# Optimization experiments

Hardware: AMD Instinct MI355X
Metric: run time of the kernel (lower is better)

Reference implementation:

```python
import jax, jax.numpy as jnp
import numpy as np

HIDDEN = 128
N_NODES = 50000
N_EDGES = 600000
EPS = 1e-5


def setup_inputs() -> dict:
    key = jax.random.key(0)
    ks = jax.random.split(key, 10)
    x = jax.random.normal(ks[0], (N_NODES, HIDDEN), dtype=jnp.float32)
    edge_index = jax.random.randint(ks[1], (2, N_EDGES), 0, N_NODES, dtype=jnp.int64)
    edge_type = jax.random.randint(ks[2], (N_EDGES,), 0, 3, dtype=jnp.int64)
    s = 0.02
    # Stacked per-type message weights: [3, 2H, H] (types 0=power, 1=comm, 2=cross)
    Wmsg = jax.random.normal(ks[3], (3, 2 * HIDDEN, HIDDEN), dtype=jnp.float32) * s
    bmsg = jnp.zeros((3, HIDDEN), dtype=jnp.float32)
    Wupd = jax.random.normal(ks[4], (2 * HIDDEN, HIDDEN), dtype=jnp.float32) * s
    bupd = jnp.zeros((HIDDEN,), dtype=jnp.float32)
    gamma = jnp.ones((HIDDEN,), dtype=jnp.float32)
    beta = jnp.zeros((HIDDEN,), dtype=jnp.float32)
    return {
        "x": x, "edge_index": edge_index, "edge_type": edge_type,
        "Wmsg": Wmsg, "bmsg": bmsg, "Wupd": Wupd, "bupd": bupd,
        "gamma": gamma, "beta": beta,
    }


def reference(x, edge_index, edge_type, Wmsg, bmsg, Wupd, bupd, gamma, beta):
    src, dst = edge_index[0], edge_index[1]
    N = x.shape[0]
    E = edge_type.shape[0]
    # Typed-edge gather + linear message: [E, 2H]
    msg_input = jnp.concatenate([x[src], x[dst]], axis=-1)
    # Compute all 3 typed linears, then select per-edge type: [E, 3, H] -> [E, H]
    all_msgs = jnp.einsum('ec,tch->eth', msg_input, Wmsg) + bmsg
    messages = jnp.take_along_axis(all_msgs, edge_type[:, None, None], axis=1)[:, 0]
    # scatter_add aggregation + count-normalize (count clamped to >= 1)
    agg = jax.ops.segment_sum(messages, dst, num_segments=N)
    count = jax.ops.segment_sum(jnp.ones((E, 1), dtype=x.dtype), dst, num_segments=N)
    agg = agg / jnp.maximum(count, 1.0)
    # Update MLP: Linear -> LayerNorm -> GELU (Dropout is identity in eval)
    h = jnp.concatenate([x, agg], axis=-1) @ Wupd + bupd
    mu = jnp.mean(h, axis=-1, keepdims=True)
    var = jnp.var(h, axis=-1, keepdims=True)
    hn = (h - mu) / jnp.sqrt(var + EPS) * gamma + beta
    x_updated = jax.nn.gelu(hn, approximate=False)
    return x + x_updated
```

## Files before the change

kernel.cpp:

```cpp
#include <hip/hip_runtime.h>
#include <hip/hip_bf16.h>
#include <math.h>

#define HIDDEN 128
#define NNODES 50000
#define NEDGES 600000
#define EPS 1e-5f
#define SCAN_CHUNK 1024
#define NSCAN_BLOCKS ((NNODES + SCAN_CHUNK - 1) / SCAN_CHUNK)
#define MPAD 50048

#define P0_W6T_END   384
#define P0_BV_END    387
#define P0_WUT_END   515
#define P0_XB_END    (515 + 6256)
#define P0_HIST_END  (P0_XB_END + 2344)

#define OFF_W6T  ((size_t)0)
#define OFF_BV   ((size_t)196608)
#define OFF_WUT  ((size_t)199680)
#define OFF_XB   ((size_t)265216)
#define OFF_ABB  ((size_t)13077504)
#define OFF_AGB  ((size_t)51477504)
#define OFF_HIST ((size_t)64289792)
#define OFF_EXCL ((size_t)64489984)
#define OFF_CURS ((size_t)64690176)
#define OFF_BSUM ((size_t)64890368)
#define OFF_PACK ((size_t)64890624)

typedef __attribute__((ext_vector_type(8))) short bf16x8;
typedef __attribute__((ext_vector_type(4))) float f32x4;

__device__ inline unsigned short f2bf(float f) {
    union { float f; unsigned u; } c; c.f = f;
    unsigned u = c.u;
    u += 0x7FFF + ((u >> 16) & 1);
    return (unsigned short)(u >> 16);
}
__device__ inline float bf2f(unsigned short h) {
    union { unsigned u; float f; } c; c.u = ((unsigned)h) << 16;
    return c.f;
}

__device__ inline unsigned char f2fp8(float f) {
    int d = __builtin_amdgcn_cvt_pk_fp8_f32(f, f, 0, false);
    return (unsigned char)(d & 0xFF);
}
template <int S>
__device__ inline float fp8f(unsigned q) {
    return __builtin_amdgcn_cvt_f32_fp8(q, S);
}

__global__ __launch_bounds__(256) void phase0(const float* __restrict__ Wmsg,
                                              const float* __restrict__ bmsg,
                                              const float* __restrict__ Wupd,
                                              const float* __restrict__ x,
                                              const int* __restrict__ ei,
                                              unsigned short* __restrict__ W6T,
                                              float* __restrict__ Bv,
                                              unsigned short* __restrict__ WuT,
                                              unsigned short* __restrict__ Xb,
                                              int* __restrict__ hist) {
    const int b = blockIdx.x;
    const int tid = threadIdx.x;
    if (b < P0_W6T_END) {
        int idx = b * 256 + tid;
        int col = idx >> 7;
        int k = idx & 127;
        int half = col >= 384;
        int rem = col - half * 384;
        int t = rem >> 7;
        int h = rem & 127;
        W6T[idx] = f2bf(Wmsg[t * 32768 + (half * 128 + k) * 128 + h]);
    } else if (b < P0_BV_END) {
        int idx = (b - P0_W6T_END) * 256 + tid;
        if (idx < 768) Bv[idx] = (idx < 384) ? 0.f : bmsg[idx - 384];
    } else if (b < P0_WUT_END) {
        int idx = (b - P0_BV_END) * 256 + tid;
        int n = idx >> 8;
        int k = idx & 255;
        WuT[idx] = f2bf(Wupd[(size_t)k * 128 + n]);
    } else if (b < P0_XB_END) {
        int i = (b - P0_WUT_END) * 256 + tid;
        int base = i * 4;
        if (base < MPAD * 128) {
            ushort4 o;
            if (base < NNODES * 128) {
                float4 v = *(const float4*)(x + base);
                o.x = f2bf(v.x); o.y = f2bf(v.y); o.z = f2bf(v.z); o.w = f2bf(v.w);
            } else {
                o.x = o.y = o.z = o.w = 0;
            }
            *(ushort4*)(Xb + base) = o;
        }
    } else {
        int e = (b - P0_XB_END) * 256 + tid;
        if (e < NEDGES) atomicAdd(&hist[ei[NEDGES + e]], 1);
    }
}

__global__ __launch_bounds__(256) void gemm_ab(const unsigned short* __restrict__ Xb,
                                               const unsigned short* __restrict__ W6T,
                                               const float* __restrict__ Bv,
                                               unsigned char* __restrict__ ABb8) {
    __shared__ unsigned char lds_buf[64 * 272];
    const int tid = threadIdx.x;
    const int mbase = blockIdx.x * 64;
    const int w = tid >> 6;
    const int nbase = blockIdx.y * 256 + w * 64;
    const int lane = tid & 63;
    const int r = lane & 15;
    const int quad = lane >> 4;

    bf16x8 b[4][4];
#pragma unroll
    for (int ks = 0; ks < 4; ++ks)
#pragma unroll
        for (int ni = 0; ni < 4; ++ni)
            b[ks][ni] = *(const bf16x8*)(W6T + (size_t)(nbase + ni * 16 + r) * 128 + ks * 32 + quad * 8);

    unsigned short* xs = (unsigned short*)lds_buf;
#pragma unroll
    for (int i = 0; i < 4; ++i) {
        int item = i * 256 + tid;
        int row = item >> 4;
        int kb = item & 15;
        bf16x8 v = *(const bf16x8*)(Xb + (size_t)(mbase + row) * 128 + kb * 8);
        *(bf16x8*)&xs[row * 128 + ((kb ^ (row & 7)) * 8)] = v;
    }
    __syncthreads();

    f32x4 acc[4][4];
#pragma unroll
    for (int mi = 0; mi < 4; ++mi)
#pragma unroll
        for (int ni = 0; ni < 4; ++ni) acc[mi][ni] = (f32x4){0.f, 0.f, 0.f, 0.f};

#pragma unroll
    for (int ks = 0; ks < 4; ++ks) {
        bf16x8 a[4];
        const int kb = ks * 4 + quad;
#pragma unroll
        for (int mi = 0; mi < 4; ++mi)
            a[mi] = *(const bf16x8*)&xs[(mi * 16 + r) * 128 + ((kb ^ (r & 7)) * 8)];
#pragma unroll
        for (int mi = 0; mi < 4; ++mi)
#pragma unroll
            for (int ni = 0; ni < 4; ++ni)
                acc[mi][ni] = __builtin_amdgcn_mfma_f32_16x16x32_bf16(a[mi], b[ks][ni], acc[mi][ni], 0, 0, 0);
    }

    __syncthreads();
    unsigned char (*tile)[272] = (unsigned char(*)[272])lds_buf;

#pragma unroll
    for (int ni = 0; ni < 4; ++ni) {
        const int col_l = w * 64 + ni * 16 + r;
        const float bias = Bv[blockIdx.y * 256 + col_l];
#pragma unroll
        for (int mi = 0; mi < 4; ++mi) {
            f32x4 v = acc[mi][ni];
#pragma unroll
            for (int reg = 0; reg < 4; ++reg) {
                tile[mi * 16 + quad * 4 + reg][col_l] = f2fp8(v[reg] + bias);
            }
        }
    }
    __syncthreads();

#pragma unroll
    for (int i = 0; i < 4; ++i) {
        int item = i * 256 + tid;
        int row_l = item >> 4;
        int chunk = item & 15;
        int grow = mbase + row_l;
        if (grow < NNODES) {
            uint4 v = *(const uint4*)&tile[row_l][chunk * 16];
            *(uint4*)(ABb8 + (size_t)grow * 768 + blockIdx.y * 256 + chunk * 16) = v;
        }
    }
}

__global__ __launch_bounds__(256) void scan_phase1(const int* __restrict__ hist,
                                                   int* __restrict__ excl,
                                                   int* __restrict__ blockSums) {
    __shared__ int lds[256];
    const int blk = blockIdx.x;
    const int t = threadIdx.x;
    const int base = blk * SCAN_CHUNK + t * 4;
    int v[4];
    int s = 0;
#pragma unroll
    for (int i = 0; i < 4; ++i) {
        v[i] = (base + i < NNODES) ? hist[base + i] : 0;
        s += v[i];
    }
    lds[t] = s;
    __syncthreads();
    for (int off = 1; off < 256; off <<= 1) {
        int add = (t >= off) ? lds[t - off] : 0;
        __syncthreads();
        lds[t] += add;
        __syncthreads();
    }
    int incl = lds[t];
    int run = incl - s;
#pragma unroll
    for (int i = 0; i < 4; ++i) {
        if (base + i < NNODES) excl[base + i] = run;
        run += v[i];
    }
    if (t == 255) blockSums[blk] = incl;
}

__global__ __launch_bounds__(256) void scan_phase3(int* __restrict__ excl,
                                                   const int* __restrict__ blockSums,
                                                   int* __restrict__ cursor) {
    __shared__ int s_add;
    const int blk = blockIdx.x;
    const int t = threadIdx.x;
    if (t < 64) {
        int v = (t < blk) ? blockSums[t] : 0;
#pragma unroll
        for (int off = 32; off >= 1; off >>= 1) v += __shfl_xor(v, off, 64);
        if (t == 0) s_add = v;
    }
    __syncthreads();
    const int add = s_add;
    for (int i = t; i < SCAN_CHUNK; i += 256) {
        int idx = blk * SCAN_CHUNK + i;
        if (idx < NNODES) {
            int o = excl[idx] + add;
            excl[idx] = o;
            cursor[idx] = o;
        }
    }
}

__global__ __launch_bounds__(256) void edge_bucket(const int* __restrict__ ei,
                                                   const int* __restrict__ et,
                                                   int* __restrict__ cursor,
                                                   unsigned* __restrict__ packed) {
    int e = blockIdx.x * 256 + threadIdx.x;
    if (e >= NEDGES) return;
    int src = ei[e];
    int dst = ei[NEDGES + e];
    int t = et[e];
    int pos = atomicAdd(&cursor[dst], 1);
    packed[pos] = (unsigned)(src * 192 + t * 32) | ((unsigned)t << 25);
}

__global__ __launch_bounds__(256) void aggregate(const unsigned* __restrict__ packed,
                                                 const int* __restrict__ excl,
                                                 const int* __restrict__ hist,
                                                 const unsigned char* __restrict__ ABb8,
                                                 unsigned short* __restrict__ Agb) {
    const int n = blockIdx.x * 4 + (threadIdx.x >> 6);
    const int lane = threadIdx.x & 63;
    if (n >= NNODES) return;
    const int start = excl[n];
    const int deg = hist[n];
    const unsigned* ABu = (const unsigned*)ABb8;

    const int half = lane >> 5;
    const int cl = lane & 31;

    float s0 = 0.f, s1 = 0.f, s2 = 0.f, s3 = 0.f;
    int c1 = 0, c2 = 0;

    for (int base = 0; base < deg; base += 64) {
        const int m = min(64, deg - base);
        unsigned v = 0;
        if (lane < m) v = packed[start + base + lane];
        int j = 0;
        for (; j + 8 <= m; j += 8) {
            unsigned e0 = __shfl(v, j + 0 + half, 64);
            unsigned e1 = __shfl(v, j + 2 + half, 64);
            unsigned e2 = __shfl(v, j + 4 + half, 64);
            unsigned e3 = __shfl(v, j + 6 + half, 64);
            unsigned q0 = ABu[(e0 & 0x1FFFFFF) + cl];
            unsigned q1 = ABu[(e1 & 0x1FFFFFF) + cl];
            unsigned q2 = ABu[(e2 & 0x1FFFFFF) + cl];
            unsigned q3 = ABu[(e3 & 0x1FFFFFF) + cl];
            int t0 = e0 >> 25, t1 = e1 >> 25, t2 = e2 >> 25, t3 = e3 >> 25;
            c1 += (t0 == 1) + (t1 == 1) + (t2 == 1) + (t3 == 1);
            c2 += (t0 == 2) + (t1 == 2) + (t2 == 2) + (t3 == 2);
            s0 += (fp8f<0>(q0) + fp8f<0>(q1)) + (fp8f<0>(q2) + fp8f<0>(q3));
            s1 += (fp8f<1>(q0) + fp8f<1>(q1)) + (fp8f<1>(q2) + fp8f<1>(q3));
            s2 += (fp8f<2>(q0) + fp8f<2>(q1)) + (fp8f<2>(q2) + fp8f<2>(q3));
            s3 += (fp8f<3>(q0) + fp8f<3>(q1)) + (fp8f<3>(q2) + fp8f<3>(q3));
        }
        for (; j + 2 <= m; j += 2) {
            unsigned e0 = __shfl(v, j + half, 64);
            unsigned q0 = ABu[(e0 & 0x1FFFFFF) + cl];
            int t0 = e0 >> 25;
            c1 += (t0 == 1);
            c2 += (t0 == 2);
            s0 += fp8f<0>(q0); s1 += fp8f<1>(q0);
            s2 += fp8f<2>(q0); s3 += fp8f<3>(q0);
        }
        if (j < m) {
            unsigned e0 = __shfl(v, j, 64);
            if (half == 0) {
                unsigned q0 = ABu[(e0 & 0x1FFFFFF) + cl];
                int t0 = e0 >> 25;
                c1 += (t0 == 1);
                c2 += (t0 == 2);
                s0 += fp8f<0>(q0); s1 += fp8f<1>(q0);
                s2 += fp8f<2>(q0); s3 += fp8f<3>(q0);
            }
        }
    }

    s0 += __shfl_xor(s0, 32, 64);
    s1 += __shfl_xor(s1, 32, 64);
    s2 += __shfl_xor(s2, 32, 64);
    s3 += __shfl_xor(s3, 32, 64);
    c1 += __shfl_xor(c1, 32, 64);
    c2 += __shfl_xor(c2, 32, 64);
    const int c0 = deg - c1 - c2;

    const unsigned* brow = ABu + (size_t)n * 192 + 96;
    if (c0) {
        unsigned p = brow[cl];
        s0 += c0 * fp8f<0>(p); s1 += c0 * fp8f<1>(p);
        s2 += c0 * fp8f<2>(p); s3 += c0 * fp8f<3>(p);
    }
    if (c1) {
        unsigned p = brow[32 + cl];
        s0 += c1 * fp8f<0>(p); s1 += c1 * fp8f<1>(p);
        s2 += c1 * fp8f<2>(p); s3 += c1 * fp8f<3>(p);
    }
    if (c2) {
        unsigned p = brow[64 + cl];
        s0 += c2 * fp8f<0>(p); s1 += c2 * fp8f<1>(p);
        s2 += c2 * fp8f<2>(p); s3 += c2 * fp8f<3>(p);
    }

    const float inv = 1.0f / fmaxf((float)deg, 1.0f);
    if (half == 0) {
        uint2 o;
        o.x = (unsigned)f2bf(s0 * inv) | ((unsigned)f2bf(s1 * inv) << 16);
        o.y = (unsigned)f2bf(s2 * inv) | ((unsigned)f2bf(s3 * inv) << 16);
        ((uint2*)(Agb + (size_t)n * 128))[cl] = o;
    }
}

__global__ __launch_bounds__(256, 4) void update_mfma(const unsigned short* __restrict__ Xb,
                                                      const unsigned short* __restrict__ Agb,
                                                      const unsigned short* __restrict__ WuT,
                                                      const float* __restrict__ bupd,
                                                      const float* __restrict__ gamma,
                                                      const float* __restrict__ beta,
                                                      float* __restrict__ out) {
    __shared__ float sred[4][2][16];

    const int tid = threadIdx.x;
    const int w = tid >> 6;
    const int lane = tid & 63;
    const int r = lane & 15;
    const int quad = lane >> 4;
    const int rowbase = blockIdx.x * 16;

    bf16x8 a[8];
#pragma unroll
    for (int ks = 0; ks < 4; ++ks)
        a[ks] = *(const bf16x8*)(Xb + (size_t)(rowbase + r) * 128 + ks * 32 + quad * 8);
#pragma unroll
    for (int ks = 4; ks < 8; ++ks)
        a[ks] = *(const bf16x8*)(Agb + (size_t)(rowbase + r) * 128 + (ks - 4) * 32 + quad * 8);

    bf16x8 e0, e1;
#pragma unroll
    for (int t = 0; t < 8; ++t) {
        e0[t] = (short)((quad * 8 + t == r) ? 0x3F80 : 0);
        e1[t] = (short)((quad * 8 + t == 16 + r) ? 0x3F80 : 0);
    }
    f32x4 xr[2];
#pragma unroll
    for (int nl = 0; nl < 2; ++nl) {
        f32x4 z = (f32x4){0.f, 0.f, 0.f, 0.f};
        xr[nl] = __builtin_amdgcn_mfma_f32_16x16x32_bf16(a[w], nl ? e1 : e0, z, 0, 0, 0);
    }

    f32x4 acc[2];
#pragma unroll
    for (int nl = 0; nl < 2; ++nl) acc[nl] = (f32x4){0.f, 0.f, 0.f, 0.f};

#pragma unroll
    for (int ks = 0; ks < 8; ++ks) {
        const int kb = ks * 4 + quad;
#pragma unroll
        for (int nl = 0; nl < 2; ++nl) {
            bf16x8 b = *(const bf16x8*)(WuT + (size_t)((w * 2 + nl) * 16 + r) * 256 + kb * 8);
            acc[nl] = __builtin_amdgcn_mfma_f32_16x16x32_bf16(a[ks], b, acc[nl], 0, 0, 0);
        }
    }

    float vals[2][4];
    float gcol[2], bcol[2];
#pragma unroll
    for (int nl = 0; nl < 2; ++nl) {
        const int col = (w * 2 + nl) * 16 + r;
        const float bias = bupd[col];
        gcol[nl] = gamma[col];
        bcol[nl] = beta[col];
#pragma unroll
        for (int reg = 0; reg < 4; ++reg) vals[nl][reg] = acc[nl][reg] + bias;
    }

#pragma unroll
    for (int reg = 0; reg < 4; ++reg) {
        float s = vals[0][reg] + vals[1][reg];
        float s2 = vals[0][reg] * vals[0][reg] + vals[1][reg] * vals[1][reg];
#pragma unroll
        for (int off = 8; off >= 1; off >>= 1) {
            s += __shfl_xor(s, off, 64);
            s2 += __shfl_xor(s2, off, 64);
        }
        if (r == 0) {
            sred[w][0][quad * 4 + reg] = s;
            sred[w][1][quad * 4 + reg] = s2;
        }
    }
    __syncthreads();

#pragma unroll
    for (int reg = 0; reg < 4; ++reg) {
        const int rowL = quad * 4 + reg;
        const float s = (sred[0][0][rowL] + sred[1][0][rowL]) + (sred[2][0][rowL] + sred[3][0][rowL]);
        const float s2 = (sred[0][1][rowL] + sred[1][1][rowL]) + (sred[2][1][rowL] + sred[3][1][rowL]);
        const int row = rowbase + rowL;
        if (row < NNODES) {
            const float mu = s * (1.0f / 128.0f);
            const float var = s2 * (1.0f / 128.0f) - mu * mu;
            const float inv = rsqrtf(var + EPS);
#pragma unroll
            for (int nl = 0; nl < 2; ++nl) {
                const int col = (w * 2 + nl) * 16 + r;
                float hn = (vals[nl][reg] - mu) * inv * gcol[nl] + bcol[nl];
                float ge = 0.5f * hn * (1.0f + erff(hn * 0.70710678118654752f));
                out[(size_t)row * 128 + col] = xr[nl][reg] + ge;
            }
        }
    }
}

extern "C" void kernel_launch(void* const* d_in, const int* in_sizes, int n_in,
                              void* d_out, int out_size, void* d_ws, size_t ws_size,
                              hipStream_t stream) {
    const float* x     = (const float*)d_in[0];
    const int*   ei    = (const int*)d_in[1];
    const int*   et    = (const int*)d_in[2];
    const float* Wmsg  = (const float*)d_in[3];
    const float* bmsg  = (const float*)d_in[4];
    const float* Wupd  = (const float*)d_in[5];
    const float* bupd  = (const float*)d_in[6];
    const float* gamma = (const float*)d_in[7];
    const float* beta  = (const float*)d_in[8];
    float* out = (float*)d_out;

    char* ws = (char*)d_ws;
    unsigned short* W6T  = (unsigned short*)(ws + OFF_W6T);
    float*          Bv   = (float*)(ws + OFF_BV);
    unsigned short* WuT  = (unsigned short*)(ws + OFF_WUT);
    unsigned short* Xb   = (unsigned short*)(ws + OFF_XB);
    unsigned char*  ABb8 = (unsigned char*)(ws + OFF_ABB);
    unsigned short* Agb  = (unsigned short*)(ws + OFF_AGB);
    int*            hist = (int*)(ws + OFF_HIST);
    int*            excl = (int*)(ws + OFF_EXCL);
    int*            curs = (int*)(ws + OFF_CURS);
    int*            bsum = (int*)(ws + OFF_BSUM);
    unsigned*       pack = (unsigned*)(ws + OFF_PACK);

    (void)hipMemsetAsync(hist, 0, NNODES * sizeof(int), stream);

    phase0<<<P0_HIST_END, 256, 0, stream>>>(Wmsg, bmsg, Wupd, x, ei, W6T, Bv, WuT, Xb, hist);
    gemm_ab<<<dim3(MPAD / 64, 3), 256, 0, stream>>>(Xb, W6T, Bv, ABb8);
    scan_phase1<<<NSCAN_BLOCKS, 256, 0, stream>>>(hist, excl, bsum);
    scan_phase3<<<NSCAN_BLOCKS, 256, 0, stream>>>(excl, bsum, curs);
    edge_bucket<<<(NEDGES + 255) / 256, 256, 0, stream>>>(ei, et, curs, pack);
    aggregate<<<(NNODES + 3) / 4, 256, 0, stream>>>(pack, excl, hist, ABb8, Agb);
    update_mfma<<<MPAD / 16, 256, 0, stream>>>(Xb, Agb, WuT, bupd, gamma, beta, out);
}
```

Before: 259.4 us.

## Make update kernel persistent with register-resident weights over 8 waves

The update GEMM+LayerNorm+GELU kernel becomes a persistent grid of 512 blocks with 512 threads. Each of the 8 waves owns one 16-column slice and keeps its Wupd^T fragment in registers, then loops over 16-row tiles. Weights and bias/gamma/beta are no longer reloaded for every tile, and a double-buffered shared reduction array allows one barrier per tile. The cost is fewer independent blocks for hiding latency and an 8-way cross-wave reduction per tile, and the A fragments are still loaded redundantly by each wave.

```diff
diff --git a/kernel.cpp b/kernel.cpp
--- a/kernel.cpp
+++ b/kernel.cpp
@@ -9,6 +9,7 @@
 #define SCAN_CHUNK 1024
 #define NSCAN_BLOCKS ((NNODES + SCAN_CHUNK - 1) / SCAN_CHUNK)
 #define MPAD 50048
+#define NTILES (MPAD / 16)
 
 #define P0_W6T_END   384
 #define P0_BV_END    387
@@ -346,101 +347,93 @@
     }
 }
 
-__global__ __launch_bounds__(256, 4) void update_mfma(const unsigned short* __restrict__ Xb,
+__global__ __launch_bounds__(512, 4) void update_mfma(const unsigned short* __restrict__ Xb,
                                                       const unsigned short* __restrict__ Agb,
                                                       const unsigned short* __restrict__ WuT,
                                                       const float* __restrict__ bupd,
                                                       const float* __restrict__ gamma,
                                                       const float* __restrict__ beta,
                                                       float* __restrict__ out) {
-    __shared__ float sred[4][2][16];
+    __shared__ float sred[2][8][2][16];
 
     const int tid = threadIdx.x;
     const int w = tid >> 6;
     const int lane = tid & 63;
     const int r = lane & 15;
     const int quad = lane >> 4;
-    const int rowbase = blockIdx.x * 16;
-
-    bf16x8 a[8];
-#pragma unroll
-    for (int ks = 0; ks < 4; ++ks)
-        a[ks] = *(const bf16x8*)(Xb + (size_t)(rowbase + r) * 128 + ks * 32 + quad * 8);
-#pragma unroll
-    for (int ks = 4; ks < 8; ++ks)
-        a[ks] = *(const bf16x8*)(Agb + (size_t)(rowbase + r) * 128 + (ks - 4) * 32 + quad * 8);
-
-    bf16x8 e0, e1;
-#pragma unroll
-    for (int t = 0; t < 8; ++t) {
-        e0[t] = (short)((quad * 8 + t == r) ? 0x3F80 : 0);
-        e1[t] = (short)((quad * 8 + t == 16 + r) ? 0x3F80 : 0);
-    }
-    f32x4 xr[2];
-#pragma unroll
-    for (int nl = 0; nl < 2; ++nl) {
-        f32x4 z = (f32x4){0.f, 0.f, 0.f, 0.f};
-        xr[nl] = __builtin_amdgcn_mfma_f32_16x16x32_bf16(a[w], nl ? e1 : e0, z, 0, 0, 0);
-    }
-
-    f32x4 acc[2];
-#pragma unroll
-    for (int nl = 0; nl < 2; ++nl) acc[nl] = (f32x4){0.f, 0.f, 0.f, 0.f};
-
-#pragma unroll
-    for (int ks = 0; ks < 8; ++ks) {
-        const int kb = ks * 4 + quad;
-#pragma unroll
-        for (int nl = 0; nl < 2; ++nl) {
-            bf16x8 b = *(const bf16x8*)(WuT + (size_t)((w * 2 + nl) * 16 + r) * 256 + kb * 8);
-            acc[nl] = __builtin_amdgcn_mfma_f32_16x16x32_bf16(a[ks], b, acc[nl], 0, 0, 0);
-        }
-    }
-
-    float vals[2][4];
-    float gcol[2], bcol[2];
-#pragma unroll
-    for (int nl = 0; nl < 2; ++nl) {
-        const int col = (w * 2 + nl) * 16 + r;
-        const float bias = bupd[col];
-        gcol[nl] = gamma[col];
-        bcol[nl] = beta[col];
-#pragma unroll
-        for (int reg = 0; reg < 4; ++reg) vals[nl][reg] = acc[nl][reg] + bias;
-    }
-
-#pragma unroll
-    for (int reg = 0; reg < 4; ++reg) {
-        float s = vals[0][reg] + vals[1][reg];
-        float s2 = vals[0][reg] * vals[0][reg] + vals[1][reg] * vals[1][reg];
-#pragma unroll
-        for (int off = 8; off >= 1; off >>= 1) {
-            s += __shfl_xor(s, off, 64);
-            s2 += __shfl_xor(s2, off, 64);
-        }
-        if (r == 0) {
-            sred[w][0][quad * 4 + reg] = s;
-            sred[w][1][quad * 4 + reg] = s2;
-        }
-    }
-    __syncthreads();
-
-#pragma unroll
-    for (int reg = 0; reg < 4; ++reg) {
-        const int rowL = quad * 4 + reg;
-        const float s = (sred[0][0][rowL] + sred[1][0][rowL]) + (sred[2][0][rowL] + sred[3][0][rowL]);
-        const float s2 = (sred[0][1][rowL] + sred[1][1][rowL]) + (sred[2][1][rowL] + sred[3][1][rowL]);
-        const int row = rowbase + rowL;
-        if (row < NNODES) {
-            const float mu = s * (1.0f / 128.0f);
-            const float var = s2 * (1.0f / 128.0f) - mu * mu;
-            const float inv = rsqrtf(var + EPS);
-#pragma unroll
-            for (int nl = 0; nl < 2; ++nl) {
-                const int col = (w * 2 + nl) * 16 + r;
-                float hn = (vals[nl][reg] - mu) * inv * gcol[nl] + bcol[nl];
+    const int col = w * 16 + r;
+
+    bf16x8 b[8];
+#pragma unroll
+    for (int ks = 0; ks < 8; ++ks)
+        b[ks] = *(const bf16x8*)(WuT + (size_t)col * 256 + (ks * 4 + quad) * 8);
+
+    const float bias = bupd[col];
+    const float gg = gamma[col];
+    const float bb = beta[col];
+
+    bf16x8 eo;
+#pragma unroll
+    for (int t = 0; t < 8; ++t)
+        eo[t] = (short)((quad * 8 + t == ((w & 1) << 4) + r) ? 0x3F80 : 0);
+
+    int p = 0;
+    for (int tile = blockIdx.x; tile < NTILES; tile += gridDim.x, p ^= 1) {
+        const int rowbase = tile * 16;
+
+        bf16x8 a[8];
+#pragma unroll
+        for (int ks = 0; ks < 4; ++ks)
+            a[ks] = *(const bf16x8*)(Xb + (size_t)(rowbase + r) * 128 + ks * 32 + quad * 8);
+#pragma unroll
+        for (int ks = 4; ks < 8; ++ks)
+            a[ks] = *(const bf16x8*)(Agb + (size_t)(rowbase + r) * 128 + (ks - 4) * 32 + quad * 8);
+
+        f32x4 acc = (f32x4){0.f, 0.f, 0.f, 0.f};
+#pragma unroll
+        for (int ks = 0; ks < 8; ++ks)
+            acc = __builtin_amdgcn_mfma_f32_16x16x32_bf16(a[ks], b[ks], acc, 0, 0, 0);
+
+        f32x4 zz = (f32x4){0.f, 0.f, 0.f, 0.f};
+        f32x4 xr = __builtin_amdgcn_mfma_f32_16x16x32_bf16(a[w >> 1], eo, zz, 0, 0, 0);
+
+        float vals[4];
+#pragma unroll
+        for (int reg = 0; reg < 4; ++reg) vals[reg] = acc[reg] + bias;
+
+#pragma unroll
+        for (int reg = 0; reg < 4; ++reg) {
+            float s = vals[reg];
+            float s2 = vals[reg] * vals[reg];
+#pragma unroll
+            for (int off = 8; off >= 1; off >>= 1) {
+                s += __shfl_xor(s, off, 64);
+                s2 += __shfl_xor(s2, off, 64);
+            }
+            if (r == 0) {
+                sred[p][w][0][quad * 4 + reg] = s;
+                sred[p][w][1][quad * 4 + reg] = s2;
+            }
+        }
+        __syncthreads();
+
+#pragma unroll
+        for (int reg = 0; reg < 4; ++reg) {
+            const int rowL = quad * 4 + reg;
+            float s = 0.f, s2 = 0.f;
+#pragma unroll
+            for (int ww = 0; ww < 8; ++ww) {
+                s += sred[p][ww][0][rowL];
+                s2 += sred[p][ww][1][rowL];
+            }
+            const int row = rowbase + rowL;
+            if (row < NNODES) {
+                const float mu = s * (1.0f / 128.0f);
+                const float var = s2 * (1.0f / 128.0f) - mu * mu;
+                const float inv = rsqrtf(var + EPS);
+                float hn = (vals[reg] - mu) * inv * gg + bb;
                 float ge = 0.5f * hn * (1.0f + erff(hn * 0.70710678118654752f));
-                out[(size_t)row * 128 + col] = xr[nl][reg] + ge;
+                out[(size_t)row * 128 + col] = xr[reg] + ge;
             }
         }
     }
@@ -481,5 +474,5 @@
     scan_phase3<<<NSCAN_BLOCKS, 256, 0, stream>>>(excl, bsum, curs);
     edge_bucket<<<(NEDGES + 255) / 256, 256, 0, stream>>>(ei, et, curs, pack);
     aggregate<<<(NNODES + 3) / 4, 256, 0, stream>>>(pack, excl, hist, ABb8, Agb);
-    update_mfma<<<MPAD / 16, 256, 0, stream>>>(Xb, Agb, WuT, bupd, gamma, beta, out);
-}
+    update_mfma<<<512, 512, 0, stream>>>(Xb, Agb, WuT, bupd, gamma, beta, out);
+}
```

New measurement: 295.5 us. 13.9% more time.
